# Kernel optimization log

Measured on AMD Instinct MI355X. Metric: run time of the kernel, lower is better.

The kernel has to match this reference:

```python
import jax, jax.numpy as jnp
import numpy as np

BATCH, D_IN, D_OUT = 2048, 1024, 4096


def setup_inputs() -> dict:
    key = jax.random.key(0)
    kx, kw = jax.random.split(key)
    x = jax.random.normal(kx, (BATCH, D_IN), dtype=jnp.float32)
    W = jax.random.normal(kw, (D_IN, D_OUT), dtype=jnp.float32)  # nn.Parameter init: N(0,1)
    return {"x": x, "W": W}


def reference(x, W):
    # out[b,o] = -1/2 * sum_i (x[b,i] - W[i,o])^2
    # instead of materializing the [B, O, I] broadcast tensor.
    x_sq = jnp.sum(x * x, axis=1, keepdims=True)          # [B, 1]
    w_sq = jnp.sum(W * W, axis=0, keepdims=True)          # [1, O]
    xw = jnp.matmul(x, W)                                  # [B, O] GEMM
    return -0.5 * (x_sq - 2.0 * xw + w_sq)
```

## Files before the change

### kernel.cpp

```cpp
#include <hip/hip_runtime.h>
#include <stdint.h>

#define BATCH 2048
#define DIN   1024
#define DOUT  4096


__device__ __forceinline__ ushort f2bf(float f) {
    uint32_t u = __float_as_uint(f);
    u += 0x7fffu + ((u >> 16) & 1u);
    return (ushort)(u >> 16);
}

__device__ __forceinline__ void async_copy16(const void* gsrc, void* ldst) {
    __builtin_amdgcn_global_load_lds(
        reinterpret_cast<uint32_t __attribute__((address_space(1)))*>(
            reinterpret_cast<uintptr_t>(gsrc)),
        reinterpret_cast<uint32_t __attribute__((address_space(3)))*>(
            reinterpret_cast<uintptr_t>(ldst)),
        16, 0, 0);
}

typedef __bf16 bf16x8 __attribute__((ext_vector_type(8)));
typedef float  f32x4  __attribute__((ext_vector_type(4)));

__global__ __launch_bounds__(256) void prep_fused(
    const float* __restrict__ x, const float* __restrict__ W,
    ushort* __restrict__ xb, ushort* __restrict__ wbt,
    float* __restrict__ xsq, float* __restrict__ wsq_part)
{
    __shared__ float smem[64 * 65 + 64];
    const int t = threadIdx.x;

    if (blockIdx.x < BATCH) {
        const int row = blockIdx.x;
        const float4 v = *(const float4*)(x + (size_t)row * DIN + t * 4);
        ushort4 pk;
        pk.x = f2bf(v.x); pk.y = f2bf(v.y); pk.z = f2bf(v.z); pk.w = f2bf(v.w);
        *(ushort4*)(xb + (size_t)row * DIN + t * 4) = pk;

        float s = v.x * v.x + v.y * v.y + v.z * v.z + v.w * v.w;
        #pragma unroll
        for (int off = 32; off > 0; off >>= 1) s += __shfl_down(s, off);
        if ((t & 63) == 0) smem[t >> 6] = s;
        __syncthreads();
        if (t == 0) xsq[row] = smem[0] + smem[1] + smem[2] + smem[3];
    } else {
        const int wblk = blockIdx.x - BATCH;
        const int o0 = (wblk & 63) * 64;
        const int i0 = (wblk >> 6) * 64;
        float (*tile)[65] = (float(*)[65])smem;
        float* csum = smem + 64 * 65;
        const int c4 = (t & 15) * 4;
        const int r0 = t >> 4;

        if (t < 64) csum[t] = 0.f;
        __syncthreads();

        float ss0 = 0.f, ss1 = 0.f, ss2 = 0.f, ss3 = 0.f;
        #pragma unroll
        for (int p = 0; p < 4; ++p) {
            const int r = r0 + p * 16;
            const float4 v = *(const float4*)&W[(size_t)(i0 + r) * DOUT + o0 + c4];
            tile[r][c4 + 0] = v.x; tile[r][c4 + 1] = v.y;
            tile[r][c4 + 2] = v.z; tile[r][c4 + 3] = v.w;
            ss0 += v.x * v.x; ss1 += v.y * v.y;
            ss2 += v.z * v.z; ss3 += v.w * v.w;
        }
        atomicAdd(&csum[c4 + 0], ss0);
        atomicAdd(&csum[c4 + 1], ss1);
        atomicAdd(&csum[c4 + 2], ss2);
        atomicAdd(&csum[c4 + 3], ss3);
        __syncthreads();
        if (t < 64) wsq_part[(size_t)(wblk >> 6) * DOUT + o0 + t] = csum[t];

        #pragma unroll
        for (int p = 0; p < 4; ++p) {
            const int orow = r0 + p * 16;
            ushort4 pk;
            pk.x = f2bf(tile[c4 + 0][orow]);
            pk.y = f2bf(tile[c4 + 1][orow]);
            pk.z = f2bf(tile[c4 + 2][orow]);
            pk.w = f2bf(tile[c4 + 3][orow]);
            *(ushort4*)&wbt[(size_t)(o0 + orow) * DIN + i0 + c4] = pk;
        }
    }
}

#define BM 128
#define BN 128
#define BK 32
#define NSTEP (DIN / BK)

__global__ __launch_bounds__(256, 2) void gemm_epi(
    const ushort* __restrict__ A,
    const ushort* __restrict__ Bt,
    const float* __restrict__ xsq,
    const float* __restrict__ wsq_part,
    float* __restrict__ out)
{
    __shared__ __align__(16) ushort sA[4][BM * BK];
    __shared__ __align__(16) ushort sB[4][BN * BK];

    const int tid  = threadIdx.x;
    const int wv   = tid >> 6;
    const int lane = tid & 63;
    const int wr = wv >> 1, wc = wv & 1;

    const int bid = blockIdx.x;
    const int xcd = bid & 7, loc = bid >> 3;
    const int bx = (xcd & 3) * 8 + (loc & 7);
    const int by = (xcd >> 2) * 8 + (loc >> 3);
    const int m0 = by * BM;
    const int n0 = bx * BN;

    const int srow = wv * 32 + (lane >> 2);
    const int scol = (((lane & 3) ^ ((lane >> 3) & 3)) << 3);
    const ushort* ag = A  + (size_t)(m0 + srow) * DIN + scol;
    const ushort* bg = Bt + (size_t)(n0 + srow) * DIN + scol;

    const int fr   = lane & 15;
    const int kq   = lane >> 4;
    const int sw   = (fr >> 1) & 3;
    const int off8 = ((kq ^ sw) << 3);
    const int arow = wr * 64 + fr;
    const int brow = wc * 64 + fr;

    f32x4 acc[4][4] = {};

    auto stage = [&](int set) {
        const int sl = set & 3;
        const int kt = set * BK;
        ushort* da = &sA[sl][wv * 1024];
        ushort* db = &sB[sl][wv * 1024];
        async_copy16(ag + kt,                 da);
        async_copy16(ag + kt + 16 * DIN,      da + 512);
        async_copy16(bg + kt,                 db);
        async_copy16(bg + kt + 16 * DIN,      db + 512);
    };

    stage(0); stage(1); stage(2);

#define K_STEP(s, vm) do {                                                    \
    asm volatile("s_waitcnt vmcnt(" #vm ")" ::: "memory");                    \
    __builtin_amdgcn_s_barrier();                                             \
    asm volatile("" ::: "memory");                                            \
    if ((s) + 3 < NSTEP) stage((s) + 3);                                      \
    const ushort* pa_ = &sA[(s) & 3][0];                                      \
    const ushort* pb_ = &sB[(s) & 3][0];                                      \
    bf16x8 fa[4], fb[4];                                                      \
    _Pragma("unroll") for (int i = 0; i < 4; ++i) {                           \
        fa[i] = *(const bf16x8*)&pa_[(arow + i * 16) * BK + off8];            \
        fb[i] = *(const bf16x8*)&pb_[(brow + i * 16) * BK + off8];            \
    }                                                                         \
    __builtin_amdgcn_s_setprio(1);                                            \
    _Pragma("unroll") for (int mi = 0; mi < 4; ++mi)                          \
    _Pragma("unroll") for (int ni = 0; ni < 4; ++ni)                          \
        acc[mi][ni] = __builtin_amdgcn_mfma_f32_16x16x32_bf16(                \
            fa[mi], fb[ni], acc[mi][ni], 0, 0, 0);                            \
    __builtin_amdgcn_s_setprio(0);                                            \
} while (0)

    #pragma unroll
    for (int s = 0; s < NSTEP - 4; ++s) K_STEP(s, 8);
    K_STEP(28, 8);
    K_STEP(29, 8);
    K_STEP(30, 4);
    K_STEP(31, 0);
#undef K_STEP

    const int er = (lane >> 4) * 4;
    const int ec = lane & 15;

    float wt[4];
    #pragma unroll
    for (int ni = 0; ni < 4; ++ni) {
        const int col = n0 + wc * 64 + ni * 16 + ec;
        float s = 0.f;
        #pragma unroll
        for (int j = 0; j < 16; ++j) s += wsq_part[(size_t)j * DOUT + col];
        wt[ni] = s;
    }

    #pragma unroll
    for (int mi = 0; mi < 4; ++mi) {
        const int row = m0 + wr * 64 + mi * 16 + er;
        #pragma unroll
        for (int ni = 0; ni < 4; ++ni) {
            const int col = n0 + wc * 64 + ni * 16 + ec;
            #pragma unroll
            for (int r = 0; r < 4; ++r) {
                out[(size_t)(row + r) * DOUT + col] =
                    acc[mi][ni][r] - 0.5f * (xsq[row + r] + wt[ni]);
            }
        }
    }
}


extern "C" void kernel_launch(void* const* d_in, const int* in_sizes, int n_in,
                              void* d_out, int out_size, void* d_ws, size_t ws_size,
                              hipStream_t stream) {
    const float* x = (const float*)d_in[0];
    const float* W = (const float*)d_in[1];
    float* out = (float*)d_out;

    char* ws = (char*)d_ws;
    ushort* xb  = (ushort*)ws;
    ushort* wbt = (ushort*)(ws + (4u << 20));
    float*  xsq = (float*)(ws + (12u << 20));
    float*  wsq_part = (float*)(ws + (12u << 20) + (16u << 10));

    prep_fused<<<BATCH + (DOUT / 64) * (DIN / 64), 256, 0, stream>>>(
        x, W, xb, wbt, xsq, wsq_part);
    gemm_epi<<<(DOUT / BN) * (BATCH / BM), 256, 0, stream>>>(
        xb, wbt, xsq, wsq_part, out);
}
```

Before: 109.2 us.

## Enlarge GEMM tile to 128x256x64 with 8 waves and triple-buffered split-phase pipeline

```diff
diff --git a/kernel.cpp b/kernel.cpp
--- a/kernel.cpp
+++ b/kernel.cpp
@@ -88,89 +88,103 @@
 }
 
 #define BM 128
-#define BN 128
-#define BK 32
-#define NSTEP (DIN / BK)
-
-__global__ __launch_bounds__(256, 2) void gemm_epi(
+#define BN 256
+#define BK 64
+#define NT (DIN / BK)
+#define SA_ELTS (BM * BK)
+#define SB_ELTS (BN * BK)
+#define LDS_BYTES ((3 * SA_ELTS + 3 * SB_ELTS) * 2)
+
+#define BARRIER() do { asm volatile("" ::: "memory");          \
+                       __builtin_amdgcn_s_barrier();           \
+                       asm volatile("" ::: "memory"); } while (0)
+
+__global__ __launch_bounds__(512, 2) void gemm_epi(
     const ushort* __restrict__ A,
     const ushort* __restrict__ Bt,
     const float* __restrict__ xsq,
     const float* __restrict__ wsq_part,
     float* __restrict__ out)
 {
-    __shared__ __align__(16) ushort sA[4][BM * BK];
-    __shared__ __align__(16) ushort sB[4][BN * BK];
+    extern __shared__ __align__(16) char smem[];
+    ushort* sAb = (ushort*)smem;
+    ushort* sBb = (ushort*)(smem + 3 * SA_ELTS * 2);
 
     const int tid  = threadIdx.x;
     const int wv   = tid >> 6;
     const int lane = tid & 63;
-    const int wr = wv >> 1, wc = wv & 1;
-
-    const int bid = blockIdx.x;
-    const int xcd = bid & 7, loc = bid >> 3;
-    const int bx = (xcd & 3) * 8 + (loc & 7);
-    const int by = (xcd >> 2) * 8 + (loc >> 3);
+    const int wr = wv >> 2, wc = wv & 3;
+
+    const int k = blockIdx.x & 7, loc = blockIdx.x >> 3;
+    const int bx = (k & 3) * 4 + (loc & 3);
+    const int by = (k >> 2) * 8 + (loc >> 2);
     const int m0 = by * BM;
     const int n0 = bx * BN;
 
-    const int srow = wv * 32 + (lane >> 2);
-    const int scol = (((lane & 3) ^ ((lane >> 3) & 3)) << 3);
+    const int srow = wv * 8 + (lane >> 3);
+    const int scol = ((lane & 7) ^ (lane >> 3)) << 3;
     const ushort* ag = A  + (size_t)(m0 + srow) * DIN + scol;
     const ushort* bg = Bt + (size_t)(n0 + srow) * DIN + scol;
 
-    const int fr   = lane & 15;
-    const int kq   = lane >> 4;
-    const int sw   = (fr >> 1) & 3;
-    const int off8 = ((kq ^ sw) << 3);
-    const int arow = wr * 64 + fr;
-    const int brow = wc * 64 + fr;
+    auto stA = [&](int b, int t, int q) {
+        async_copy16(ag + (size_t)t * BK + (size_t)q * 64 * DIN,
+                     sAb + (size_t)b * SA_ELTS + (wv * 8 + q * 64) * BK);
+    };
+    auto stB = [&](int b, int t, int q) {
+        async_copy16(bg + (size_t)t * BK + (size_t)q * 64 * DIN,
+                     sBb + (size_t)b * SB_ELTS + (wv * 8 + q * 64) * BK);
+    };
+
+    const int fr = lane & 15, q4 = lane >> 4, fr7 = lane & 7;
+    const int cks[2] = { (q4 ^ fr7) << 3, ((4 + q4) ^ fr7) << 3 };
+    const int arow0 = wr * 64 + fr;
+    const int brow0 = wc * 64 + fr;
 
     f32x4 acc[4][4] = {};
 
-    auto stage = [&](int set) {
-        const int sl = set & 3;
-        const int kt = set * BK;
-        ushort* da = &sA[sl][wv * 1024];
-        ushort* db = &sB[sl][wv * 1024];
-        async_copy16(ag + kt,                 da);
-        async_copy16(ag + kt + 16 * DIN,      da + 512);
-        async_copy16(bg + kt,                 db);
-        async_copy16(bg + kt + 16 * DIN,      db + 512);
-    };
-
-    stage(0); stage(1); stage(2);
-
-#define K_STEP(s, vm) do {                                                    \
-    asm volatile("s_waitcnt vmcnt(" #vm ")" ::: "memory");                    \
-    __builtin_amdgcn_s_barrier();                                             \
-    asm volatile("" ::: "memory");                                            \
-    if ((s) + 3 < NSTEP) stage((s) + 3);                                      \
-    const ushort* pa_ = &sA[(s) & 3][0];                                      \
-    const ushort* pb_ = &sB[(s) & 3][0];                                      \
-    bf16x8 fa[4], fb[4];                                                      \
-    _Pragma("unroll") for (int i = 0; i < 4; ++i) {                           \
-        fa[i] = *(const bf16x8*)&pa_[(arow + i * 16) * BK + off8];            \
-        fb[i] = *(const bf16x8*)&pb_[(brow + i * 16) * BK + off8];            \
-    }                                                                         \
-    __builtin_amdgcn_s_setprio(1);                                            \
-    _Pragma("unroll") for (int mi = 0; mi < 4; ++mi)                          \
-    _Pragma("unroll") for (int ni = 0; ni < 4; ++ni)                          \
-        acc[mi][ni] = __builtin_amdgcn_mfma_f32_16x16x32_bf16(                \
-            fa[mi], fb[ni], acc[mi][ni], 0, 0, 0);                            \
-    __builtin_amdgcn_s_setprio(0);                                            \
+#define PHASE(CUR, KS, STAGE, CLOSE) do {                                   \
+    const ushort* pa_ = sAb + (CUR) * SA_ELTS;                              \
+    const ushort* pb_ = sBb + (CUR) * SB_ELTS;                              \
+    bf16x8 fa[4], fb[4];                                                    \
+    _Pragma("unroll") for (int i = 0; i < 4; ++i)                           \
+        fa[i] = *(const bf16x8*)&pa_[(arow0 + i * 16) * BK + cks[KS]];      \
+    _Pragma("unroll") for (int i = 0; i < 4; ++i)                           \
+        fb[i] = *(const bf16x8*)&pb_[(brow0 + i * 16) * BK + cks[KS]];      \
+    STAGE;                                                                  \
+    BARRIER();                                                              \
+    __builtin_amdgcn_s_setprio(1);                                          \
+    _Pragma("unroll") for (int mi = 0; mi < 4; ++mi)                        \
+    _Pragma("unroll") for (int ni = 0; ni < 4; ++ni)                        \
+        acc[mi][ni] = __builtin_amdgcn_mfma_f32_16x16x32_bf16(              \
+            fa[mi], fb[ni], acc[mi][ni], 0, 0, 0);                          \
+    __builtin_amdgcn_s_setprio(0);                                          \
+    CLOSE;                                                                  \
+    BARRIER();                                                              \
 } while (0)
 
+    stA(0, 0, 0); stA(0, 0, 1);
+    stB(0, 0, 0); stB(0, 0, 1); stB(0, 0, 2); stB(0, 0, 3);
+    stA(1, 1, 0); stA(1, 1, 1);
+    stB(1, 1, 0); stB(1, 1, 1); stB(1, 1, 2); stB(1, 1, 3);
+    asm volatile("s_waitcnt vmcnt(6)" ::: "memory");
+    BARRIER();
+
     #pragma unroll
-    for (int s = 0; s < NSTEP - 4; ++s) K_STEP(s, 8);
-    K_STEP(28, 8);
-    K_STEP(29, 8);
-    K_STEP(30, 4);
-    K_STEP(31, 0);
-#undef K_STEP
-
-    const int er = (lane >> 4) * 4;
-    const int ec = lane & 15;
+    for (int s = 0; s < NT - 2; ++s) {
+        const int cur = s % 3, n3 = (s + 2) % 3, t2 = s + 2;
+        PHASE(cur, 0, (stA(n3, t2, 0), stA(n3, t2, 1), stB(n3, t2, 0)),
+              (void)0);
+        PHASE(cur, 1, (stB(n3, t2, 1), stB(n3, t2, 2), stB(n3, t2, 3)),
+              asm volatile("s_waitcnt vmcnt(6)" ::: "memory"));
+    }
+    PHASE(2, 0, (void)0, (void)0);
+    PHASE(2, 1, (void)0, asm volatile("s_waitcnt vmcnt(0)" ::: "memory"));
+    PHASE(0, 0, (void)0, (void)0);
+    PHASE(0, 1, (void)0, (void)0);
+#undef PHASE
+
+    const int er = q4 * 4;
+    const int ec = fr;
 
     float wt[4];
     #pragma unroll
@@ -211,8 +225,16 @@
     float*  xsq = (float*)(ws + (12u << 20));
     float*  wsq_part = (float*)(ws + (12u << 20) + (16u << 10));
 
+    static bool attr_done = false;
+    if (!attr_done) {
+        hipFuncSetAttribute((const void*)gemm_epi,
+                            hipFuncAttributeMaxDynamicSharedMemorySize,
+                            LDS_BYTES);
+        attr_done = true;
+    }
+
     prep_fused<<<BATCH + (DOUT / 64) * (DIN / 64), 256, 0, stream>>>(
         x, W, xb, wbt, xsq, wsq_part);
-    gemm_epi<<<(DOUT / BN) * (BATCH / BM), 256, 0, stream>>>(
+    gemm_epi<<<(DOUT / BN) * (BATCH / BM), 512, LDS_BYTES, stream>>>(
         xb, wbt, xsq, wsq_part, out);
 }
```

New measurement: 106.3 us. 1.03x faster.
